# Optimization experiments

Hardware: AMD Instinct MI355X
Metric: run time of the kernel (lower is better)

Reference implementation:

```python
import jax, jax.numpy as jnp
import numpy as np

B, T, D, H = 2, 2048, 1024, 16
DH = D // H


def setup_inputs() -> dict:
    key = jax.random.key(0)
    k1, k2, k3 = jax.random.split(key, 3)
    x = jax.random.normal(k1, (B, T, D), dtype=jnp.float32)
    # causal mask: True at positions to mask (strict upper triangle)
    attn_mask = jnp.triu(jnp.ones((T, T), dtype=bool), k=1)
    attn_mask = jnp.broadcast_to(attn_mask, (B, T, T))
    Wqkv = jax.random.normal(k2, (D, 3 * D), dtype=jnp.float32) * (D ** -0.5)
    Wo = jax.random.normal(k3, (D, D), dtype=jnp.float32) * (D ** -0.5)
    bo = jnp.zeros((D,), dtype=jnp.float32)
    return {"x": x, "attn_mask": attn_mask, "Wqkv": Wqkv, "Wo": Wo, "bo": bo}


def reference(x, attn_mask, Wqkv, Wo, bo):
    # qkv projection (bias=False), split into q,k,v like torch chunk(3, dim=-1)
    qkv = x @ Wqkv                                  # [B,T,3D]
    q, k, v = jnp.split(qkv, 3, axis=-1)            # each [B,T,D]
    q = q.reshape(B, T, H, DH).transpose(0, 2, 1, 3)  # [B,H,T,DH]
    k = k.reshape(B, T, H, DH).transpose(0, 2, 1, 3)
    v = v.reshape(B, T, H, DH).transpose(0, 2, 1, 3)
    scores = jnp.einsum('bhqd,bhkd->bhqk', q, k) / jnp.sqrt(jnp.float32(DH))
    scores = jnp.where(attn_mask[:, None, :, :], -jnp.inf, scores)
    weights = jax.nn.softmax(scores, axis=-1)       # [B,H,T,T]
    out = jnp.einsum('bhqk,bhkd->bhqd', weights, v)  # [B,H,T,DH]
    out = out.transpose(0, 2, 1, 3).reshape(B, T, D)
    out = out @ Wo + bo                              # o_proj
    # dropout is identity in eval mode
    return (out, weights)
```

## Files before the change

### kernel.cpp

```cpp
#include <hip/hip_runtime.h>
#include <hip/hip_bf16.h>


typedef __attribute__((ext_vector_type(8))) short short8;
typedef __attribute__((ext_vector_type(4))) float floatx4;

__device__ inline unsigned short f2bf(float f) {
  union { float f; unsigned u; } x; x.f = f;
  unsigned r = x.u + 0x7fffu + ((x.u >> 16) & 1u);
  return (unsigned short)(r >> 16);
}

__global__ __launch_bounds__(256) void convert_x_kernel(
    const float* __restrict__ src, unsigned short* __restrict__ dst, int n4) {
  int i = blockIdx.x * 256 + threadIdx.x;
  int stride = gridDim.x * 256;
  for (; i < n4; i += stride) {
    float4 v = ((const float4*)src)[i];
    ushort4 o;
    o.x = f2bf(v.x); o.y = f2bf(v.y); o.z = f2bf(v.z); o.w = f2bf(v.w);
    ((ushort4*)dst)[i] = o;
  }
}

__global__ __launch_bounds__(256) void tconv_kernel(
    const float* __restrict__ src, unsigned short* __restrict__ dst,
    int R, int C) {
  __shared__ float tile[32][33];
  int c0 = blockIdx.x * 32, r0 = blockIdx.y * 32;
  int tr = threadIdx.x >> 5, tc = threadIdx.x & 31;
#pragma unroll
  for (int i = 0; i < 4; ++i) {
    int r = tr + i * 8;
    tile[r][tc] = src[(size_t)(r0 + r) * C + c0 + tc];
  }
  __syncthreads();
#pragma unroll
  for (int i = 0; i < 4; ++i) {
    int r = tr + i * 8;
    dst[(size_t)(c0 + r) * R + r0 + tc] = f2bf(tile[tc][r]);
  }
}

__global__ __launch_bounds__(256) void gemm_qkv_kernel(
    const unsigned short* __restrict__ A,
    const unsigned short* __restrict__ Bt,
    unsigned short* __restrict__ qb, unsigned short* __restrict__ kb,
    unsigned short* __restrict__ vtb) {
  __shared__ __align__(16) unsigned short As[128][32];
  __shared__ __align__(16) unsigned short Bs[128][32];
  const int tid = threadIdx.x;
  const int w = tid >> 6, lane = tid & 63, quad = lane >> 4, l15 = lane & 15;
  const int wm = (w >> 1) * 64, wn = (w & 1) * 64;
  const int m0 = blockIdx.y * 128, n0 = blockIdx.x * 128;
  floatx4 acc[4][4] = {};
  for (int k0 = 0; k0 < 1024; k0 += 32) {
    __syncthreads();
#pragma unroll
    for (int it = 0; it < 2; ++it) {
      int s = tid + it * 256;
      int r = s >> 2, seg = s & 3;
      *(uint4*)&As[r][seg * 8] =
          *(const uint4*)(A + (size_t)(m0 + r) * 1024 + k0 + seg * 8);
      *(uint4*)&Bs[r][seg * 8] =
          *(const uint4*)(Bt + (size_t)(n0 + r) * 1024 + k0 + seg * 8);
    }
    __syncthreads();
    short8 a[4], b[4];
#pragma unroll
    for (int i = 0; i < 4; ++i) a[i] = *(const short8*)&As[wm + i * 16 + l15][quad * 8];
#pragma unroll
    for (int j = 0; j < 4; ++j) b[j] = *(const short8*)&Bs[wn + j * 16 + l15][quad * 8];
#pragma unroll
    for (int i = 0; i < 4; ++i)
#pragma unroll
      for (int j = 0; j < 4; ++j)
        acc[i][j] = __builtin_amdgcn_mfma_f32_16x16x32_bf16(a[i], b[j], acc[i][j], 0, 0, 0);
  }
  const int sel = n0 >> 10;
#pragma unroll
  for (int i = 0; i < 4; ++i) {
    int m = m0 + wm + i * 16 + quad * 4;
    int bb = m >> 11, t = m & 2047;
    if (sel < 2) {
      unsigned short* dst = (sel == 0) ? qb : kb;
#pragma unroll
      for (int j = 0; j < 4; ++j) {
        int n = n0 + wn + j * 16 + l15;
        int h = (n & 1023) >> 6, dh = n & 63;
        int bh = bb * 16 + h;
#pragma unroll
        for (int r = 0; r < 4; ++r)
          dst[((size_t)bh * 2048 + t + r) * 64 + dh] = f2bf(acc[i][j][r]);
      }
    } else {
#pragma unroll
      for (int j = 0; j < 4; ++j) {
        int n = n0 + wn + j * 16 + l15;
        int h = (n & 1023) >> 6, dh = n & 63;
        int bh = bb * 16 + h;
        ushort4 p;
        p.x = f2bf(acc[i][j][0]); p.y = f2bf(acc[i][j][1]);
        p.z = f2bf(acc[i][j][2]); p.w = f2bf(acc[i][j][3]);
        *(ushort4*)&vtb[((size_t)bh * 64 + dh) * 2048 + t] = p;
      }
    }
  }
}

__global__ __launch_bounds__(256) void attn_kernel(
    const unsigned short* __restrict__ qb, const unsigned short* __restrict__ kb,
    const unsigned short* __restrict__ vtb,
    float* __restrict__ wout,
    unsigned short* __restrict__ attnb) {
  __shared__ __align__(16) unsigned short Qs[64][64];
  __shared__ __align__(16) unsigned short Ks[64][64];
  __shared__ __align__(16) unsigned short Vs[64][64];
  __shared__ __align__(16) unsigned short Es[64][64];
  const int tid = threadIdx.x;
  const int w = tid >> 6, lane = tid & 63, quad = lane >> 4, l15 = lane & 15;
  const int bh = blockIdx.x >> 5;
  const int qt = 31 - (blockIdx.x & 31);
  const size_t kvbase = (size_t)bh * 131072;

  {
    int nz4 = (31 - qt) * 16;
    if (nz4 > 0) {
      float4 z4 = make_float4(0.f, 0.f, 0.f, 0.f);
      float4* wbase = (float4*)(wout + ((size_t)(bh * 2048 + qt * 64)) * 2048 + (qt + 1) * 64);
      for (int r = 0; r < 64; ++r) {
        float4* row = wbase + (size_t)r * 512;
        for (int c4 = tid; c4 < nz4; c4 += 256) row[c4] = z4;
      }
    }
  }
#pragma unroll
  for (int it = 0; it < 2; ++it) {
    int s = tid + it * 256, r = s >> 3, c8 = s & 7;
    *(uint4*)&Qs[r][c8 * 8] =
        *(const uint4*)(qb + kvbase + (size_t)(qt * 64 + r) * 64 + c8 * 8);
  }
  __syncthreads();
  const short8 aq0 = *(const short8*)&Qs[w * 16 + l15][quad * 8];
  const short8 aq1 = *(const short8*)&Qs[w * 16 + l15][quad * 8 + 32];

  float sums[4] = {0.f, 0.f, 0.f, 0.f};
  for (int kt = 0; kt <= qt; ++kt) {
    __syncthreads();
#pragma unroll
    for (int it = 0; it < 2; ++it) {
      int s = tid + it * 256, r = s >> 3, c8 = s & 7;
      *(uint4*)&Ks[r][c8 * 8] =
          *(const uint4*)(kb + kvbase + (size_t)(kt * 64 + r) * 64 + c8 * 8);
    }
    __syncthreads();
#pragma unroll
    for (int c = 0; c < 4; ++c) {
      short8 b0 = *(const short8*)&Ks[c * 16 + l15][quad * 8];
      short8 b1 = *(const short8*)&Ks[c * 16 + l15][quad * 8 + 32];
      floatx4 d = {0.f, 0.f, 0.f, 0.f};
      d = __builtin_amdgcn_mfma_f32_16x16x32_bf16(aq0, b0, d, 0, 0, 0);
      d = __builtin_amdgcn_mfma_f32_16x16x32_bf16(aq1, b1, d, 0, 0, 0);
      int col = c * 16 + l15;
      int rowb = w * 16 + quad * 4;
      if (kt == qt) {
#pragma unroll
        for (int r = 0; r < 4; ++r)
          sums[r] += (col <= rowb + r) ? __expf(d[r] * 0.125f) : 0.f;
      } else {
#pragma unroll
        for (int r = 0; r < 4; ++r) sums[r] += __expf(d[r] * 0.125f);
      }
    }
  }
  float rinv[4];
#pragma unroll
  for (int r = 0; r < 4; ++r) {
    float s = sums[r];
    s += __shfl_xor(s, 1); s += __shfl_xor(s, 2);
    s += __shfl_xor(s, 4); s += __shfl_xor(s, 8);
    rinv[r] = 1.f / s;
  }

  floatx4 oacc[4] = {};
  const size_t wrowbase = ((size_t)(bh * 2048 + qt * 64 + w * 16 + quad * 4)) * 2048;
  for (int kt = 0; kt <= qt; ++kt) {
    __syncthreads();
#pragma unroll
    for (int it = 0; it < 2; ++it) {
      int s = tid + it * 256, r = s >> 3, c8 = s & 7;
      *(uint4*)&Ks[r][c8 * 8] =
          *(const uint4*)(kb + kvbase + (size_t)(kt * 64 + r) * 64 + c8 * 8);
      *(uint4*)&Vs[r][c8 * 8] =
          *(const uint4*)(vtb + kvbase + (size_t)r * 2048 + kt * 64 + c8 * 8);
    }
    __syncthreads();
#pragma unroll
    for (int c = 0; c < 4; ++c) {
      short8 b0 = *(const short8*)&Ks[c * 16 + l15][quad * 8];
      short8 b1 = *(const short8*)&Ks[c * 16 + l15][quad * 8 + 32];
      floatx4 d = {0.f, 0.f, 0.f, 0.f};
      d = __builtin_amdgcn_mfma_f32_16x16x32_bf16(aq0, b0, d, 0, 0, 0);
      d = __builtin_amdgcn_mfma_f32_16x16x32_bf16(aq1, b1, d, 0, 0, 0);
      int col = c * 16 + l15;
      int rowb = w * 16 + quad * 4;
#pragma unroll
      for (int r = 0; r < 4; ++r) {
        float ev = __expf(d[r] * 0.125f);
        if (kt == qt && col > rowb + r) ev = 0.f;
        wout[wrowbase + (size_t)r * 2048 + kt * 64 + col] = ev * rinv[r];
        Es[rowb + r][col] = f2bf(ev);
      }
    }
    short8 ae0 = *(const short8*)&Es[w * 16 + l15][quad * 8];
    short8 ae1 = *(const short8*)&Es[w * 16 + l15][quad * 8 + 32];
#pragma unroll
    for (int c = 0; c < 4; ++c) {
      short8 bv0 = *(const short8*)&Vs[c * 16 + l15][quad * 8];
      short8 bv1 = *(const short8*)&Vs[c * 16 + l15][quad * 8 + 32];
      oacc[c] = __builtin_amdgcn_mfma_f32_16x16x32_bf16(ae0, bv0, oacc[c], 0, 0, 0);
      oacc[c] = __builtin_amdgcn_mfma_f32_16x16x32_bf16(ae1, bv1, oacc[c], 0, 0, 0);
    }
  }
  const int bb = bh >> 4, h = bh & 15;
#pragma unroll
  for (int c = 0; c < 4; ++c)
#pragma unroll
    for (int r = 0; r < 4; ++r) {
      int q = qt * 64 + w * 16 + quad * 4 + r;
      attnb[((size_t)bb * 2048 + q) * 1024 + h * 64 + c * 16 + l15] =
          f2bf(oacc[c][r] * rinv[r]);
    }
}

__global__ __launch_bounds__(256) void gemm_o_kernel(
    const unsigned short* __restrict__ A,
    const unsigned short* __restrict__ Bt,
    const float* __restrict__ bo,
    float* __restrict__ out) {
  __shared__ __align__(16) unsigned short As[128][32];
  __shared__ __align__(16) unsigned short Bs[128][32];
  const int tid = threadIdx.x;
  const int w = tid >> 6, lane = tid & 63, quad = lane >> 4, l15 = lane & 15;
  const int wm = (w >> 1) * 64, wn = (w & 1) * 64;
  const int m0 = blockIdx.y * 128, n0 = blockIdx.x * 128;
  floatx4 acc[4][4] = {};
  for (int k0 = 0; k0 < 1024; k0 += 32) {
    __syncthreads();
#pragma unroll
    for (int it = 0; it < 2; ++it) {
      int s = tid + it * 256;
      int r = s >> 2, seg = s & 3;
      *(uint4*)&As[r][seg * 8] =
          *(const uint4*)(A + (size_t)(m0 + r) * 1024 + k0 + seg * 8);
      *(uint4*)&Bs[r][seg * 8] =
          *(const uint4*)(Bt + (size_t)(n0 + r) * 1024 + k0 + seg * 8);
    }
    __syncthreads();
    short8 a[4], b[4];
#pragma unroll
    for (int i = 0; i < 4; ++i) a[i] = *(const short8*)&As[wm + i * 16 + l15][quad * 8];
#pragma unroll
    for (int j = 0; j < 4; ++j) b[j] = *(const short8*)&Bs[wn + j * 16 + l15][quad * 8];
#pragma unroll
    for (int i = 0; i < 4; ++i)
#pragma unroll
      for (int j = 0; j < 4; ++j)
        acc[i][j] = __builtin_amdgcn_mfma_f32_16x16x32_bf16(a[i], b[j], acc[i][j], 0, 0, 0);
  }
#pragma unroll
  for (int i = 0; i < 4; ++i) {
    int m = m0 + wm + i * 16 + quad * 4;
#pragma unroll
    for (int j = 0; j < 4; ++j) {
      int n = n0 + wn + j * 16 + l15;
      float bias = bo[n];
#pragma unroll
      for (int r = 0; r < 4; ++r)
        out[(size_t)(m + r) * 1024 + n] = acc[i][j][r] + bias;
    }
  }
}

extern "C" void kernel_launch(void* const* d_in, const int* in_sizes, int n_in,
                              void* d_out, int out_size, void* d_ws, size_t ws_size,
                              hipStream_t stream) {
  const float* x    = (const float*)d_in[0];
  const float* wqkv = (const float*)d_in[2];
  const float* wo   = (const float*)d_in[3];
  const float* bo   = (const float*)d_in[4];
  float* out  = (float*)d_out;
  float* wout = out + 4194304;

  unsigned short* xb    = (unsigned short*)d_ws;
  unsigned short* wqkvT = xb + 4194304;
  unsigned short* woT   = wqkvT + 3145728;
  unsigned short* qb    = woT + 1048576;
  unsigned short* kb    = qb + 4194304;
  unsigned short* vtb   = kb + 4194304;
  unsigned short* attnb = vtb + 4194304;

  convert_x_kernel<<<1024, 256, 0, stream>>>(x, xb, 1048576);
  tconv_kernel<<<dim3(96, 32), 256, 0, stream>>>(wqkv, wqkvT, 1024, 3072);
  tconv_kernel<<<dim3(32, 32), 256, 0, stream>>>(wo, woT, 1024, 1024);
  gemm_qkv_kernel<<<dim3(24, 32), 256, 0, stream>>>(xb, wqkvT, qb, kb, vtb);
  attn_kernel<<<1024, 256, 0, stream>>>(qb, kb, vtb, wout, attnb);
  gemm_o_kernel<<<dim3(8, 32), 256, 0, stream>>>(attnb, woT, bo, out);
}
```

Baseline: 775.9 us.

## Swizzle Q/K/V layouts, use direct global-to-LDS loads, pair causal tiles per block

The QKV GEMM now writes Q, K and transposed V with an XOR swizzle on 8-element chunks, and the attention kernel reads LDS with matching XOR indexing to avoid bank conflicts. Global-to-shared copies in all GEMM and attention loops use the global_load_lds builtin, which skips the round trip through registers. The attention grid is halved and each block processes query tiles j and 31-j so causal work is balanced across blocks. Writes of the weights matrix and its zero fill use nontemporal stores. The gains depend on the swizzle and load-to-LDS semantics being exactly right, and fewer blocks means less parallelism.

```diff
diff --git a/kernel.cpp b/kernel.cpp
--- a/kernel.cpp
+++ b/kernel.cpp
@@ -4,6 +4,13 @@
 
 typedef __attribute__((ext_vector_type(8))) short short8;
 typedef __attribute__((ext_vector_type(4))) float floatx4;
+
+typedef __attribute__((address_space(1))) const unsigned int gas_u32;
+typedef __attribute__((address_space(3))) unsigned int las_u32;
+
+__device__ inline void gl16(const void* g, void* l) {
+  __builtin_amdgcn_global_load_lds((gas_u32*)g, (las_u32*)l, 16, 0, 0);
+}
 
 __device__ inline unsigned short f2bf(float f) {
   union { float f; unsigned u; } x; x.f = f;
@@ -60,10 +67,8 @@
     for (int it = 0; it < 2; ++it) {
       int s = tid + it * 256;
       int r = s >> 2, seg = s & 3;
-      *(uint4*)&As[r][seg * 8] =
-          *(const uint4*)(A + (size_t)(m0 + r) * 1024 + k0 + seg * 8);
-      *(uint4*)&Bs[r][seg * 8] =
-          *(const uint4*)(Bt + (size_t)(n0 + r) * 1024 + k0 + seg * 8);
+      gl16(A + (size_t)(m0 + r) * 1024 + k0 + seg * 8, &As[r][seg * 8]);
+      gl16(Bt + (size_t)(n0 + r) * 1024 + k0 + seg * 8, &Bs[r][seg * 8]);
     }
     __syncthreads();
     short8 a[4], b[4];
@@ -90,8 +95,11 @@
         int h = (n & 1023) >> 6, dh = n & 63;
         int bh = bb * 16 + h;
 #pragma unroll
-        for (int r = 0; r < 4; ++r)
-          dst[((size_t)bh * 2048 + t + r) * 64 + dh] = f2bf(acc[i][j][r]);
+        for (int r = 0; r < 4; ++r) {
+          int trow = t + r;
+          int swdh = ((((dh >> 3) ^ (trow & 7)) << 3)) | (dh & 7);
+          dst[((size_t)bh * 2048 + trow) * 64 + swdh] = f2bf(acc[i][j][r]);
+        }
       }
     } else {
 #pragma unroll
@@ -102,7 +110,8 @@
         ushort4 p;
         p.x = f2bf(acc[i][j][0]); p.y = f2bf(acc[i][j][1]);
         p.z = f2bf(acc[i][j][2]); p.w = f2bf(acc[i][j][3]);
-        *(ushort4*)&vtb[((size_t)bh * 64 + dh) * 2048 + t] = p;
+        int swoff = (((((t & 63) >> 3) ^ (dh & 7)) << 3)) | (t & 7);
+        *(ushort4*)&vtb[((size_t)bh * 64 + dh) * 2048 + (t & ~63) + swoff] = p;
       }
     }
   }
@@ -119,118 +128,122 @@
   __shared__ __align__(16) unsigned short Es[64][64];
   const int tid = threadIdx.x;
   const int w = tid >> 6, lane = tid & 63, quad = lane >> 4, l15 = lane & 15;
-  const int bh = blockIdx.x >> 5;
-  const int qt = 31 - (blockIdx.x & 31);
+  const int bh = blockIdx.x >> 4;
+  const int j = blockIdx.x & 15;
   const size_t kvbase = (size_t)bh * 131072;
-
-  {
-    int nz4 = (31 - qt) * 16;
-    if (nz4 > 0) {
-      float4 z4 = make_float4(0.f, 0.f, 0.f, 0.f);
-      float4* wbase = (float4*)(wout + ((size_t)(bh * 2048 + qt * 64)) * 2048 + (qt + 1) * 64);
-      for (int r = 0; r < 64; ++r) {
-        float4* row = wbase + (size_t)r * 512;
-        for (int c4 = tid; c4 < nz4; c4 += 256) row[c4] = z4;
-      }
-    }
-  }
-#pragma unroll
-  for (int it = 0; it < 2; ++it) {
-    int s = tid + it * 256, r = s >> 3, c8 = s & 7;
-    *(uint4*)&Qs[r][c8 * 8] =
-        *(const uint4*)(qb + kvbase + (size_t)(qt * 64 + r) * 64 + c8 * 8);
-  }
-  __syncthreads();
-  const short8 aq0 = *(const short8*)&Qs[w * 16 + l15][quad * 8];
-  const short8 aq1 = *(const short8*)&Qs[w * 16 + l15][quad * 8 + 32];
-
-  float sums[4] = {0.f, 0.f, 0.f, 0.f};
-  for (int kt = 0; kt <= qt; ++kt) {
-    __syncthreads();
+  const int key = l15 & 7;
+  const int rowb = w * 16 + quad * 4;
+
+  for (int half = 0; half < 2; ++half) {
+    const int qt = half ? j : (31 - j);
+
+    {
+      int nz4 = (31 - qt) * 16;
+      if (nz4 > 0) {
+        floatx4 z4 = {0.f, 0.f, 0.f, 0.f};
+        floatx4* wbase = (floatx4*)(wout + ((size_t)(bh * 2048 + qt * 64)) * 2048 + (qt + 1) * 64);
+        for (int r = 0; r < 64; ++r) {
+          floatx4* row = wbase + (size_t)r * 512;
+          for (int c4 = tid; c4 < nz4; c4 += 256)
+            __builtin_nontemporal_store(z4, row + c4);
+        }
+      }
+    }
 #pragma unroll
     for (int it = 0; it < 2; ++it) {
       int s = tid + it * 256, r = s >> 3, c8 = s & 7;
-      *(uint4*)&Ks[r][c8 * 8] =
-          *(const uint4*)(kb + kvbase + (size_t)(kt * 64 + r) * 64 + c8 * 8);
-    }
-    __syncthreads();
-#pragma unroll
-    for (int c = 0; c < 4; ++c) {
-      short8 b0 = *(const short8*)&Ks[c * 16 + l15][quad * 8];
-      short8 b1 = *(const short8*)&Ks[c * 16 + l15][quad * 8 + 32];
-      floatx4 d = {0.f, 0.f, 0.f, 0.f};
-      d = __builtin_amdgcn_mfma_f32_16x16x32_bf16(aq0, b0, d, 0, 0, 0);
-      d = __builtin_amdgcn_mfma_f32_16x16x32_bf16(aq1, b1, d, 0, 0, 0);
-      int col = c * 16 + l15;
-      int rowb = w * 16 + quad * 4;
-      if (kt == qt) {
-#pragma unroll
-        for (int r = 0; r < 4; ++r)
-          sums[r] += (col <= rowb + r) ? __expf(d[r] * 0.125f) : 0.f;
-      } else {
-#pragma unroll
-        for (int r = 0; r < 4; ++r) sums[r] += __expf(d[r] * 0.125f);
-      }
-    }
-  }
-  float rinv[4];
-#pragma unroll
-  for (int r = 0; r < 4; ++r) {
-    float s = sums[r];
-    s += __shfl_xor(s, 1); s += __shfl_xor(s, 2);
-    s += __shfl_xor(s, 4); s += __shfl_xor(s, 8);
-    rinv[r] = 1.f / s;
-  }
-
-  floatx4 oacc[4] = {};
-  const size_t wrowbase = ((size_t)(bh * 2048 + qt * 64 + w * 16 + quad * 4)) * 2048;
-  for (int kt = 0; kt <= qt; ++kt) {
-    __syncthreads();
-#pragma unroll
-    for (int it = 0; it < 2; ++it) {
-      int s = tid + it * 256, r = s >> 3, c8 = s & 7;
-      *(uint4*)&Ks[r][c8 * 8] =
-          *(const uint4*)(kb + kvbase + (size_t)(kt * 64 + r) * 64 + c8 * 8);
-      *(uint4*)&Vs[r][c8 * 8] =
-          *(const uint4*)(vtb + kvbase + (size_t)r * 2048 + kt * 64 + c8 * 8);
-    }
-    __syncthreads();
-#pragma unroll
-    for (int c = 0; c < 4; ++c) {
-      short8 b0 = *(const short8*)&Ks[c * 16 + l15][quad * 8];
-      short8 b1 = *(const short8*)&Ks[c * 16 + l15][quad * 8 + 32];
-      floatx4 d = {0.f, 0.f, 0.f, 0.f};
-      d = __builtin_amdgcn_mfma_f32_16x16x32_bf16(aq0, b0, d, 0, 0, 0);
-      d = __builtin_amdgcn_mfma_f32_16x16x32_bf16(aq1, b1, d, 0, 0, 0);
-      int col = c * 16 + l15;
-      int rowb = w * 16 + quad * 4;
+      gl16(qb + kvbase + (size_t)(qt * 64 + r) * 64 + c8 * 8, &Qs[r][c8 * 8]);
+    }
+    __syncthreads();
+    const short8 aq0 = *(const short8*)&Qs[w * 16 + l15][(quad ^ key) << 3];
+    const short8 aq1 = *(const short8*)&Qs[w * 16 + l15][((quad + 4) ^ key) << 3];
+
+    float sums[4] = {0.f, 0.f, 0.f, 0.f};
+    for (int kt = 0; kt <= qt; ++kt) {
+      __syncthreads();
+#pragma unroll
+      for (int it = 0; it < 2; ++it) {
+        int s = tid + it * 256, r = s >> 3, c8 = s & 7;
+        gl16(kb + kvbase + (size_t)(kt * 64 + r) * 64 + c8 * 8, &Ks[r][c8 * 8]);
+      }
+      __syncthreads();
+#pragma unroll
+      for (int c = 0; c < 4; ++c) {
+        short8 b0 = *(const short8*)&Ks[c * 16 + l15][(quad ^ key) << 3];
+        short8 b1 = *(const short8*)&Ks[c * 16 + l15][((quad + 4) ^ key) << 3];
+        floatx4 d = {0.f, 0.f, 0.f, 0.f};
+        d = __builtin_amdgcn_mfma_f32_16x16x32_bf16(aq0, b0, d, 0, 0, 0);
+        d = __builtin_amdgcn_mfma_f32_16x16x32_bf16(aq1, b1, d, 0, 0, 0);
+        int col = c * 16 + l15;
+        if (kt == qt) {
+#pragma unroll
+          for (int r = 0; r < 4; ++r)
+            sums[r] += (col <= rowb + r) ? __expf(d[r] * 0.125f) : 0.f;
+        } else {
+#pragma unroll
+          for (int r = 0; r < 4; ++r) sums[r] += __expf(d[r] * 0.125f);
+        }
+      }
+    }
+    float rinv[4];
+#pragma unroll
+    for (int r = 0; r < 4; ++r) {
+      float s = sums[r];
+      s += __shfl_xor(s, 1); s += __shfl_xor(s, 2);
+      s += __shfl_xor(s, 4); s += __shfl_xor(s, 8);
+      rinv[r] = 1.f / s;
+    }
+
+    floatx4 oacc[4] = {};
+    const size_t wrowbase = ((size_t)(bh * 2048 + qt * 64 + rowb)) * 2048;
+    for (int kt = 0; kt <= qt; ++kt) {
+      __syncthreads();
+#pragma unroll
+      for (int it = 0; it < 2; ++it) {
+        int s = tid + it * 256, r = s >> 3, c8 = s & 7;
+        gl16(kb + kvbase + (size_t)(kt * 64 + r) * 64 + c8 * 8, &Ks[r][c8 * 8]);
+        gl16(vtb + kvbase + (size_t)r * 2048 + kt * 64 + c8 * 8, &Vs[r][c8 * 8]);
+      }
+      __syncthreads();
+#pragma unroll
+      for (int c = 0; c < 4; ++c) {
+        short8 b0 = *(const short8*)&Ks[c * 16 + l15][(quad ^ key) << 3];
+        short8 b1 = *(const short8*)&Ks[c * 16 + l15][((quad + 4) ^ key) << 3];
+        floatx4 d = {0.f, 0.f, 0.f, 0.f};
+        d = __builtin_amdgcn_mfma_f32_16x16x32_bf16(aq0, b0, d, 0, 0, 0);
+        d = __builtin_amdgcn_mfma_f32_16x16x32_bf16(aq1, b1, d, 0, 0, 0);
+        int col = c * 16 + l15;
+#pragma unroll
+        for (int r = 0; r < 4; ++r) {
+          float ev = __expf(d[r] * 0.125f);
+          if (kt == qt && col > rowb + r) ev = 0.f;
+          __builtin_nontemporal_store(ev * rinv[r],
+              wout + wrowbase + (size_t)r * 2048 + kt * 64 + col);
+          int erow = rowb + r;
+          int sc = (((col >> 3) ^ (erow & 7)) << 3) | (col & 7);
+          Es[erow][sc] = f2bf(ev);
+        }
+      }
+      const short8 ae0 = *(const short8*)&Es[w * 16 + l15][(quad ^ key) << 3];
+      const short8 ae1 = *(const short8*)&Es[w * 16 + l15][((quad + 4) ^ key) << 3];
+#pragma unroll
+      for (int c = 0; c < 4; ++c) {
+        short8 bv0 = *(const short8*)&Vs[c * 16 + l15][(quad ^ key) << 3];
+        short8 bv1 = *(const short8*)&Vs[c * 16 + l15][((quad + 4) ^ key) << 3];
+        oacc[c] = __builtin_amdgcn_mfma_f32_16x16x32_bf16(ae0, bv0, oacc[c], 0, 0, 0);
+        oacc[c] = __builtin_amdgcn_mfma_f32_16x16x32_bf16(ae1, bv1, oacc[c], 0, 0, 0);
+      }
+    }
+    const int bb = bh >> 4, h = bh & 15;
+#pragma unroll
+    for (int c = 0; c < 4; ++c)
 #pragma unroll
       for (int r = 0; r < 4; ++r) {
-        float ev = __expf(d[r] * 0.125f);
-        if (kt == qt && col > rowb + r) ev = 0.f;
-        wout[wrowbase + (size_t)r * 2048 + kt * 64 + col] = ev * rinv[r];
-        Es[rowb + r][col] = f2bf(ev);
-      }
-    }
-    short8 ae0 = *(const short8*)&Es[w * 16 + l15][quad * 8];
-    short8 ae1 = *(const short8*)&Es[w * 16 + l15][quad * 8 + 32];
-#pragma unroll
-    for (int c = 0; c < 4; ++c) {
-      short8 bv0 = *(const short8*)&Vs[c * 16 + l15][quad * 8];
-      short8 bv1 = *(const short8*)&Vs[c * 16 + l15][quad * 8 + 32];
-      oacc[c] = __builtin_amdgcn_mfma_f32_16x16x32_bf16(ae0, bv0, oacc[c], 0, 0, 0);
-      oacc[c] = __builtin_amdgcn_mfma_f32_16x16x32_bf16(ae1, bv1, oacc[c], 0, 0, 0);
-    }
-  }
-  const int bb = bh >> 4, h = bh & 15;
-#pragma unroll
-  for (int c = 0; c < 4; ++c)
-#pragma unroll
-    for (int r = 0; r < 4; ++r) {
-      int q = qt * 64 + w * 16 + quad * 4 + r;
-      attnb[((size_t)bb * 2048 + q) * 1024 + h * 64 + c * 16 + l15] =
-          f2bf(oacc[c][r] * rinv[r]);
-    }
+        int q = qt * 64 + w * 16 + quad * 4 + r;
+        attnb[((size_t)bb * 2048 + q) * 1024 + h * 64 + c * 16 + l15] =
+            f2bf(oacc[c][r] * rinv[r]);
+      }
+  }
 }
 
 __global__ __launch_bounds__(256) void gemm_o_kernel(
@@ -251,10 +264,8 @@
     for (int it = 0; it < 2; ++it) {
       int s = tid + it * 256;
       int r = s >> 2, seg = s & 3;
-      *(uint4*)&As[r][seg * 8] =
-          *(const uint4*)(A + (size_t)(m0 + r) * 1024 + k0 + seg * 8);
-      *(uint4*)&Bs[r][seg * 8] =
-          *(const uint4*)(Bt + (size_t)(n0 + r) * 1024 + k0 + seg * 8);
+      gl16(A + (size_t)(m0 + r) * 1024 + k0 + seg * 8, &As[r][seg * 8]);
+      gl16(Bt + (size_t)(n0 + r) * 1024 + k0 + seg * 8, &Bs[r][seg * 8]);
     }
     __syncthreads();
     short8 a[4], b[4];
@@ -304,6 +315,6 @@
   tconv_kernel<<<dim3(96, 32), 256, 0, stream>>>(wqkv, wqkvT, 1024, 3072);
   tconv_kernel<<<dim3(32, 32), 256, 0, stream>>>(wo, woT, 1024, 1024);
   gemm_qkv_kernel<<<dim3(24, 32), 256, 0, stream>>>(xb, wqkvT, qb, kb, vtb);
-  attn_kernel<<<1024, 256, 0, stream>>>(qb, kb, vtb, wout, attnb);
+  attn_kernel<<<512, 256, 0, stream>>>(qb, kb, vtb, wout, attnb);
   gemm_o_kernel<<<dim3(8, 32), 256, 0, stream>>>(attnb, woT, bo, out);
 }
```

After: 755.9 us. 1.03x faster.
